# Performance work log

Hardware: AMD Instinct MI355X
Metric: run time of the kernel (lower is better)

The kernel has to match this reference:

```python
import jax, jax.numpy as jnp
import numpy as np

B, H, W, C_IN = 16, 32, 32, 2048
C_PROJ = 2048          # hard-coded Conv2D filters in the module
D_Q = 512              # queries last dim
A = 64                 # num_attributes


def setup_inputs() -> dict:
    key = jax.random.key(0)
    ks = jax.random.split(key, 8)
    s = lambda fan_in: 1.0 / np.sqrt(fan_in)
    return {
        "queries": jax.random.normal(ks[0], (B, C_PROJ, D_Q), jnp.float32),
        "features": jax.random.normal(ks[1], (B, H, W, C_IN), jnp.float32),
        # Dense(num_attributes) on queries
        "Wq": jax.random.normal(ks[2], (D_Q, A), jnp.float32) * s(D_Q),
        "bq": jnp.zeros((A,), jnp.float32),
        # Conv2D 1x1 -> 2048 (feature_transform)
        "Wf": jax.random.normal(ks[3], (C_IN, C_PROJ), jnp.float32) * s(C_IN),
        "bf": jnp.zeros((C_PROJ,), jnp.float32),
        # Conv2D 1x1 -> 2048 (feature_transform1)
        "Wf1": jax.random.normal(ks[4], (C_IN, C_PROJ), jnp.float32) * s(C_IN),
        "bf1": jnpp if False else jnp.zeros((C_PROJ,), jnp.float32),
    }


def reference(queries, features, Wq, bq, Wf, bf, Wf1, bf1):
    # Q: [B, C_PROJ, A]
    Q = jnp.einsum("bcd,da->bca", queries, Wq) + bq
    # 1x1 convs are per-pixel linear maps: [B, H, W, C_PROJ]
    F = jnp.einsum("bhwc,cf->bhwf", features, Wf) + bf
    S = jnp.einsum("bhwc,cf->bhwf", features, Wf1) + bf1
    b, h, w, c = F.shape
    F_new = F.reshape(b, h * w, c)                      # [B, HW, C]
    scale = 1.0 / jnp.sqrt(jnp.float32(A))
    # scores: [B, HW, A]; softmax over attribute axis
    attn = jax.nn.softmax(jnp.einsum("bnc,bca->bna", F_new, Q) * scale, axis=-1)
    attention_map = attn.reshape(b, h, w, A)
    S_flat = S.reshape(b, h * w, c)                     # [B, HW, C]
    # readout: S^T @ attn -> [B, C, A]
    out = jnp.einsum("bnc,bna->bca", S_flat, attn)
    return attention_map, out
```

## Files before the change

kernel.cpp:

```cpp
#include <hip/hip_runtime.h>
#include <math.h>


#define CCH 2048
#define HWD 1024
#define BAD 1024
#define DQD 512
#define NA  64

typedef __attribute__((ext_vector_type(8))) short bf16x8;
typedef __attribute__((ext_vector_type(4))) float f32x4;
typedef __attribute__((ext_vector_type(4))) unsigned short us4;
typedef __attribute__((ext_vector_type(8))) unsigned short us8;

__device__ __forceinline__ unsigned short bfhi(float v) {
    return (unsigned short)(__float_as_uint(v) >> 16);
}
__device__ __forceinline__ float bfres(float v) {
    return v - __uint_as_float(__float_as_uint(v) & 0xffff0000u);
}
__device__ __forceinline__ float bf2f(unsigned short h) {
    return __uint_as_float(((unsigned)h) << 16);
}

__global__ __launch_bounds__(256) void k_convWq(const float* __restrict__ Wq,
    unsigned short* __restrict__ hi, unsigned short* __restrict__ lo)
{
    __shared__ float t[64][65];
    const int tid = threadIdx.x;
    const int k0 = blockIdx.x * 64;
#pragma unroll
    for (int r = 0; r < 4; ++r) {
        int kr = (tid >> 4) + r * 16;
        int cc = (tid & 15) * 4;
        float4 v = *(const float4*)&Wq[(size_t)(k0 + kr) * NA + cc];
        t[kr][cc] = v.x; t[kr][cc + 1] = v.y; t[kr][cc + 2] = v.z; t[kr][cc + 3] = v.w;
    }
    __syncthreads();
#pragma unroll
    for (int r = 0; r < 2; ++r) {
        int a = (tid >> 3) + r * 32;
        int g = tid & 7;
        us8 h8, l8;
#pragma unroll
        for (int j = 0; j < 8; ++j) {
            float v = t[g * 8 + j][a];
            h8[j] = bfhi(v); l8[j] = bfhi(bfres(v));
        }
        *(us8*)&hi[(size_t)a * DQD + k0 + g * 8] = h8;
        *(us8*)&lo[(size_t)a * DQD + k0 + g * 8] = l8;
    }
}

template <int EPI>
__global__ __launch_bounds__(256) void k_gemm_A32(
    const float* __restrict__ A,
    const unsigned short* __restrict__ Bh, const unsigned short* __restrict__ Bl,
    const float* __restrict__ bias,
    unsigned short* __restrict__ Oh, unsigned short* __restrict__ Ol,
    int K, int ldb)
{
    __shared__ unsigned short AsH[4][64][8], AsL[4][64][8], BsH[4][64][8], BsL[4][64][8];
    const int tid = threadIdx.x;
    const int m0 = blockIdx.x * 64, gy = blockIdx.y;
    const int w = tid >> 6, l = tid & 63, lr = l & 15, lg = l >> 4;
    const int sm = tid >> 2, sk = tid & 3, kq = sk * 4;

    const float* pA = A + (size_t)(m0 + sm) * K;
    const unsigned short* pBh = Bh + (size_t)(gy * 64 + sm) * ldb + sk * 8;
    const unsigned short* pBl = Bl + (size_t)(gy * 64 + sm) * ldb + sk * 8;

    f32x4 acc[4] = {{0.f,0.f,0.f,0.f},{0.f,0.f,0.f,0.f},{0.f,0.f,0.f,0.f},{0.f,0.f,0.f,0.f}};

    for (int k0 = 0; k0 < K; k0 += 32) {
        float4 a0 = *(const float4*)&pA[k0 + kq];
        float4 a1 = *(const float4*)&pA[k0 + 16 + kq];
        uint4 vbh = *(const uint4*)pBh; uint4 vbl = *(const uint4*)pBl;
        pBh += 32; pBl += 32;
        us4 h0, l0, h1, l1;
        float a0r[4] = {a0.x, a0.y, a0.z, a0.w}, a1r[4] = {a1.x, a1.y, a1.z, a1.w};
#pragma unroll
        for (int j = 0; j < 4; ++j) {
            h0[j] = bfhi(a0r[j]); l0[j] = bfhi(bfres(a0r[j]));
            h1[j] = bfhi(a1r[j]); l1[j] = bfhi(bfres(a1r[j]));
        }
        __syncthreads();
        *(us4*)&AsH[kq >> 3][sm][kq & 7] = h0;
        *(us4*)&AsL[kq >> 3][sm][kq & 7] = l0;
        *(us4*)&AsH[2 + (kq >> 3)][sm][kq & 7] = h1;
        *(us4*)&AsL[2 + (kq >> 3)][sm][kq & 7] = l1;
        *(uint4*)&BsH[sk][sm][0] = vbh;
        *(uint4*)&BsL[sk][sm][0] = vbl;
        __syncthreads();
        bf16x8 afh = *(const bf16x8*)&AsH[lg][w * 16 + lr][0];
        bf16x8 afl = *(const bf16x8*)&AsL[lg][w * 16 + lr][0];
#pragma unroll
        for (int nt = 0; nt < 4; ++nt) {
            bf16x8 bfh = *(const bf16x8*)&BsH[lg][nt * 16 + lr][0];
            bf16x8 bfl = *(const bf16x8*)&BsL[lg][nt * 16 + lr][0];
            acc[nt] = __builtin_amdgcn_mfma_f32_16x16x32_bf16(afh, bfh, acc[nt], 0, 0, 0);
            acc[nt] = __builtin_amdgcn_mfma_f32_16x16x32_bf16(afh, bfl, acc[nt], 0, 0, 0);
            acc[nt] = __builtin_amdgcn_mfma_f32_16x16x32_bf16(afl, bfh, acc[nt], 0, 0, 0);
        }
    }

    const int mrow0 = m0 + w * 16 + lg * 4;
    if (EPI == 0) {
#pragma unroll
        for (int nt = 0; nt < 4; ++nt) {
            int nn = gy * 64 + nt * 16 + lr;
            us4 h, lo;
#pragma unroll
            for (int j = 0; j < 4; ++j) {
                float v = acc[nt][j];
                h[j] = bfhi(v); lo[j] = bfhi(bfres(v));
            }
            *(us4*)&Oh[(size_t)nn * CCH + mrow0] = h;
            *(us4*)&Ol[(size_t)nn * CCH + mrow0] = lo;
        }
    } else {
        const int b = mrow0 >> 11, cp = mrow0 & 2047;
#pragma unroll
        for (int nt = 0; nt < 4; ++nt) {
            int nloc = nt * 16 + lr;
            float bb = bias[nloc];
            int row = b * 64 + nloc;
            us4 h, lo;
#pragma unroll
            for (int j = 0; j < 4; ++j) {
                float v = acc[nt][j] + bb;
                h[j] = bfhi(v); lo[j] = bfhi(bfres(v));
            }
            *(us4*)&Oh[(size_t)row * CCH + cp] = h;
            *(us4*)&Ol[(size_t)row * CCH + cp] = lo;
        }
    }
}

__global__ __launch_bounds__(256) void k_bq(const unsigned short* __restrict__ QTh,
    const unsigned short* __restrict__ QTl, const float* __restrict__ bf,
    float* __restrict__ bQ)
{
    const int row = blockIdx.x, tid = threadIdx.x;
    us8 h = *(const us8*)(QTh + (size_t)row * CCH + tid * 8);
    us8 l = *(const us8*)(QTl + (size_t)row * CCH + tid * 8);
    float s = 0.f;
#pragma unroll
    for (int j = 0; j < 8; ++j)
        s = fmaf(bf2f(h[j]) + bf2f(l[j]), bf[tid * 8 + j], s);
#pragma unroll
    for (int off = 1; off < 64; off <<= 1) s += __shfl_xor(s, off);
    __shared__ float ps[4];
    if ((tid & 63) == 0) ps[tid >> 6] = s;
    __syncthreads();
    if (tid == 0) bQ[row] = ps[0] + ps[1] + ps[2] + ps[3];
}

__global__ __launch_bounds__(256) void k_scores(
    const float* __restrict__ feat,
    const unsigned short* __restrict__ FQh, const unsigned short* __restrict__ FQl,
    const float* __restrict__ bQ, float* __restrict__ attn,
    unsigned short* __restrict__ ATh, unsigned short* __restrict__ ATl)
{
    __shared__ unsigned short AsH[4][64][8], AsL[4][64][8], BsH[4][64][8], BsL[4][64][8];
    const int tid = threadIdx.x;
    const int b = blockIdx.y, n0 = blockIdx.x * 64;
    const int w = tid >> 6, l = tid & 63, lr = l & 15, lg = l >> 4;
    const int sm = tid >> 2, sk = tid & 3, kq = sk * 4;

    const float* fb = feat + ((size_t)b * HWD + n0) * CCH;
    const unsigned short* pBh = FQh + (size_t)(b * 64 + sm) * CCH + sk * 8;
    const unsigned short* pBl = FQl + (size_t)(b * 64 + sm) * CCH + sk * 8;

    f32x4 acc[4] = {{0.f,0.f,0.f,0.f},{0.f,0.f,0.f,0.f},{0.f,0.f,0.f,0.f},{0.f,0.f,0.f,0.f}};

    for (int k0 = 0; k0 < CCH; k0 += 32) {
        float4 a0 = *(const float4*)&fb[(size_t)sm * CCH + k0 + kq];
        float4 a1 = *(const float4*)&fb[(size_t)sm * CCH + k0 + 16 + kq];
        uint4 vbh = *(const uint4*)pBh; uint4 vbl = *(const uint4*)pBl;
        pBh += 32; pBl += 32;
        us4 h0, l0, h1, l1;
        float a0r[4] = {a0.x, a0.y, a0.z, a0.w}, a1r[4] = {a1.x, a1.y, a1.z, a1.w};
#pragma unroll
        for (int j = 0; j < 4; ++j) {
            h0[j] = bfhi(a0r[j]); l0[j] = bfhi(bfres(a0r[j]));
            h1[j] = bfhi(a1r[j]); l1[j] = bfhi(bfres(a1r[j]));
        }
        __syncthreads();
        *(us4*)&AsH[kq >> 3][sm][kq & 7] = h0;
        *(us4*)&AsL[kq >> 3][sm][kq & 7] = l0;
        *(us4*)&AsH[2 + (kq >> 3)][sm][kq & 7] = h1;
        *(us4*)&AsL[2 + (kq >> 3)][sm][kq & 7] = l1;
        *(uint4*)&BsH[sk][sm][0] = vbh;
        *(uint4*)&BsL[sk][sm][0] = vbl;
        __syncthreads();
        bf16x8 afh = *(const bf16x8*)&AsH[lg][w * 16 + lr][0];
        bf16x8 afl = *(const bf16x8*)&AsL[lg][w * 16 + lr][0];
#pragma unroll
        for (int nt = 0; nt < 4; ++nt) {
            bf16x8 bfh = *(const bf16x8*)&BsH[lg][nt * 16 + lr][0];
            bf16x8 bfl = *(const bf16x8*)&BsL[lg][nt * 16 + lr][0];
            acc[nt] = __builtin_amdgcn_mfma_f32_16x16x32_bf16(afh, bfh, acc[nt], 0, 0, 0);
            acc[nt] = __builtin_amdgcn_mfma_f32_16x16x32_bf16(afh, bfl, acc[nt], 0, 0, 0);
            acc[nt] = __builtin_amdgcn_mfma_f32_16x16x32_bf16(afl, bfh, acc[nt], 0, 0, 0);
        }
    }

    float bq4[4];
#pragma unroll
    for (int nt = 0; nt < 4; ++nt) bq4[nt] = bQ[b * NA + nt * 16 + lr];
#pragma unroll
    for (int j = 0; j < 4; ++j) {
        float v[4];
#pragma unroll
        for (int nt = 0; nt < 4; ++nt) v[nt] = (acc[nt][j] + bq4[nt]) * 0.125f;
        float m = fmaxf(fmaxf(v[0], v[1]), fmaxf(v[2], v[3]));
        m = fmaxf(m, __shfl_xor(m, 1));
        m = fmaxf(m, __shfl_xor(m, 2));
        m = fmaxf(m, __shfl_xor(m, 4));
        m = fmaxf(m, __shfl_xor(m, 8));
        float e[4], s = 0.f;
#pragma unroll
        for (int nt = 0; nt < 4; ++nt) { e[nt] = expf(v[nt] - m); s += e[nt]; }
        s += __shfl_xor(s, 1);
        s += __shfl_xor(s, 2);
        s += __shfl_xor(s, 4);
        s += __shfl_xor(s, 8);
        float inv = 1.f / s;
        const int nr = n0 + w * 16 + lg * 4 + j;
#pragma unroll
        for (int nt = 0; nt < 4; ++nt) {
            float av = e[nt] * inv;
            attn[((size_t)b * HWD + nr) * NA + nt * 16 + lr] = av;
            size_t trow = (size_t)(b * 64 + nt * 16 + lr) * HWD + nr;
            ATh[trow] = bfhi(av);
            ATl[trow] = bfhi(bfres(av));
        }
    }
}

__global__ __launch_bounds__(256) void k_lsum1(const float* __restrict__ attn,
                                               float* __restrict__ part)
{
    const int g = blockIdx.x, b = blockIdx.y;
    const int a = threadIdx.x & 63, q = threadIdx.x >> 6;
    float s = 0.f;
#pragma unroll 4
    for (int n = g * 64 + q * 16; n < g * 64 + q * 16 + 16; ++n)
        s += attn[((size_t)b * HWD + n) * NA + a];
    __shared__ float p[4][64];
    p[q][a] = s;
    __syncthreads();
    if (q == 0) part[(size_t)g * BAD + b * NA + a] = p[0][a] + p[1][a] + p[2][a] + p[3][a];
}

__global__ __launch_bounds__(64) void k_lsum2(const float* __restrict__ part,
                                              float* __restrict__ L)
{
    int ba = blockIdx.x * 64 + threadIdx.x;
    float s = 0.f;
#pragma unroll
    for (int g = 0; g < 16; ++g) s += part[(size_t)g * BAD + ba];
    L[ba] = s;
}

template <int EPI>
__global__ __launch_bounds__(256) void k_gemm_T(
    const float* __restrict__ G,
    const unsigned short* __restrict__ Bh, const unsigned short* __restrict__ Bl,
    unsigned short* __restrict__ Oh, unsigned short* __restrict__ Ol,
    float* __restrict__ Ofp, const float* __restrict__ bias, const float* __restrict__ Lv,
    int K, int ldg, int ldb, long gslab)
{
    __shared__ float At[2048];
    __shared__ unsigned short BsH[4][64][8], BsL[4][64][8];
    const int tid = threadIdx.x;
    const int m0 = blockIdx.x * 64, gy = blockIdx.y;
    const int w = tid >> 6, l = tid & 63, lr = l & 15, lg = l >> 4;
    const int sm = tid >> 2, sk = tid & 3;
    const int kr = tid >> 3, c8 = (tid & 7) * 8;
    const int wkey = (kr >> 3) << 4;
    const int acol = ((w ^ lg) << 4) | lr;

    const float* Gb = G + (size_t)gy * gslab;
    const unsigned short* pBh = Bh + (size_t)(gy * 64 + sm) * ldb + sk * 8;
    const unsigned short* pBl = Bl + (size_t)(gy * 64 + sm) * ldb + sk * 8;

    f32x4 acc[4] = {{0.f,0.f,0.f,0.f},{0.f,0.f,0.f,0.f},{0.f,0.f,0.f,0.f},{0.f,0.f,0.f,0.f}};

    for (int k0 = 0; k0 < K; k0 += 32) {
        float4 g0 = *(const float4*)&Gb[(size_t)(k0 + kr) * ldg + m0 + c8];
        float4 g1 = *(const float4*)&Gb[(size_t)(k0 + kr) * ldg + m0 + c8 + 4];
        uint4 vbh = *(const uint4*)pBh; uint4 vbl = *(const uint4*)pBl;
        pBh += 32; pBl += 32;
        __syncthreads();
        *(float4*)&At[kr * 64 + (c8 ^ wkey)] = g0;
        *(float4*)&At[kr * 64 + (c8 ^ wkey) + 4] = g1;
        *(uint4*)&BsH[sk][sm][0] = vbh;
        *(uint4*)&BsL[sk][sm][0] = vbl;
        __syncthreads();
        bf16x8 afh, afl;
#pragma unroll
        for (int j = 0; j < 8; ++j) {
            float v = At[(lg * 8 + j) * 64 + acol];
            afh[j] = (short)bfhi(v);
            afl[j] = (short)bfhi(bfres(v));
        }
#pragma unroll
        for (int nt = 0; nt < 4; ++nt) {
            bf16x8 bfh = *(const bf16x8*)&BsH[lg][nt * 16 + lr][0];
            bf16x8 bfl = *(const bf16x8*)&BsL[lg][nt * 16 + lr][0];
            acc[nt] = __builtin_amdgcn_mfma_f32_16x16x32_bf16(afh, bfh, acc[nt], 0, 0, 0);
            acc[nt] = __builtin_amdgcn_mfma_f32_16x16x32_bf16(afh, bfl, acc[nt], 0, 0, 0);
            acc[nt] = __builtin_amdgcn_mfma_f32_16x16x32_bf16(afl, bfh, acc[nt], 0, 0, 0);
        }
    }

    const int mrow0 = m0 + w * 16 + lg * 4;
    if (EPI == 0) {
#pragma unroll
        for (int nt = 0; nt < 4; ++nt) {
            int nn = gy * 64 + nt * 16 + lr;
            us4 h, lo;
#pragma unroll
            for (int j = 0; j < 4; ++j) {
                float v = acc[nt][j];
                h[j] = bfhi(v); lo[j] = bfhi(bfres(v));
            }
            *(us4*)&Oh[(size_t)nn * CCH + mrow0] = h;
            *(us4*)&Ol[(size_t)nn * CCH + mrow0] = lo;
        }
    } else {
        float bv[4];
#pragma unroll
        for (int j = 0; j < 4; ++j) bv[j] = bias[mrow0 + j];
#pragma unroll
        for (int nt = 0; nt < 4; ++nt) {
            int nn = gy * 64 + nt * 16 + lr;
            float lb = Lv[nn];
            size_t base = (size_t)(nn >> 6) * (CCH * NA) + (size_t)(nn & 63);
#pragma unroll
            for (int j = 0; j < 4; ++j)
                Ofp[base + (size_t)(mrow0 + j) * NA] = fmaf(bv[j], lb, acc[nt][j]);
        }
    }
}

extern "C" void kernel_launch(void* const* d_in, const int* in_sizes, int n_in,
                              void* d_out, int out_size, void* d_ws, size_t ws_size,
                              hipStream_t stream)
{
    (void)in_sizes; (void)n_in; (void)out_size; (void)ws_size;
    const float* queries  = (const float*)d_in[0];
    const float* features = (const float*)d_in[1];
    const float* Wq  = (const float*)d_in[2];
    const float* bq  = (const float*)d_in[3];
    const float* Wf  = (const float*)d_in[4];
    const float* bf  = (const float*)d_in[5];
    const float* Wf1 = (const float*)d_in[6];
    const float* bf1 = (const float*)d_in[7];
    float* out = (float*)d_out;
    char*  W   = (char*)d_ws;

    unsigned short* QTh = (unsigned short*)(W);
    unsigned short* QTl = (unsigned short*)(W + (4u << 20));
    unsigned short* FQh = (unsigned short*)(W + (8u << 20));
    unsigned short* FQl = (unsigned short*)(W + (12u << 20));
    unsigned short* WqTh = (unsigned short*)(W + (16u << 20));
    unsigned short* WqTl = (unsigned short*)(W + (16u << 20) + (64u << 10));
    float* bQ   = (float*)(W + (16u << 20) + (128u << 10));
    float* L    = (float*)(W + (16u << 20) + (128u << 10) + 4096);
    float* part = (float*)(W + (16u << 20) + (128u << 10) + 8192);
    unsigned short* ATh = QTh;
    unsigned short* ATl = (unsigned short*)(W + (2u << 20));
    unsigned short* TTh = FQh;
    unsigned short* TTl = FQl;

    float* attn = out;
    float* outm = out + 1048576;

    k_convWq<<<dim3(8), 256, 0, stream>>>(Wq, WqTh, WqTl);
    k_gemm_A32<1><<<dim3(512, 1), 256, 0, stream>>>(queries, WqTh, WqTl, bq, QTh, QTl,
                                                    DQD, DQD);
    k_bq<<<dim3(1024), 256, 0, stream>>>(QTh, QTl, bf, bQ);
    k_gemm_A32<0><<<dim3(32, 16), 256, 0, stream>>>(Wf, QTh, QTl, nullptr, FQh, FQl,
                                                    CCH, CCH);
    k_scores<<<dim3(16, 16), 256, 0, stream>>>(features, FQh, FQl, bQ, attn, ATh, ATl);
    k_lsum1<<<dim3(16, 16), 256, 0, stream>>>(attn, part);
    k_lsum2<<<dim3(16), 64, 0, stream>>>(part, L);
    k_gemm_T<0><<<dim3(32, 16), 256, 0, stream>>>(features, ATh, ATl, TTh, TTl,
                                                  nullptr, nullptr, nullptr,
                                                  HWD, CCH, HWD, (long)HWD * CCH);
    k_gemm_T<1><<<dim3(32, 16), 256, 0, stream>>>(Wf1, TTh, TTl, nullptr, nullptr,
                                                  outm, bf1, L,
                                                  CCH, CCH, CCH, 0L);
}
```

Baseline: 489.1 us.

## Restructure GEMM pipeline with pre-split weights, split-K, and separate softmax

Every GEMM stage is rewritten. Wf and Wf1 are converted to hi/lo bf16 up front, and Wf1 is also transposed. The big weight GEMMs now use split-K into fp32 partials, loading operands directly from global memory without LDS, with small combine kernels afterwards. The scores GEMM is split along K, and the softmax plus the attention transpose and sum moves into its own kernel. The T GEMM uses a double-buffered LDS tile with smaller tiles to raise occupancy. The aim is to cut the per-iteration conversion work and barrier syncs and to put more blocks in flight, at the cost of extra partial-buffer traffic and more kernel launches.

```diff
diff --git a/kernel.cpp b/kernel.cpp
--- a/kernel.cpp
+++ b/kernel.cpp
@@ -4,7 +4,6 @@
 
 #define CCH 2048
 #define HWD 1024
-#define BAD 1024
 #define DQD 512
 #define NA  64
 
@@ -21,6 +20,50 @@
 }
 __device__ __forceinline__ float bf2f(unsigned short h) {
     return __uint_as_float(((unsigned)h) << 16);
+}
+
+#define MFMA(A, B, C) __builtin_amdgcn_mfma_f32_16x16x32_bf16((A), (B), (C), 0, 0, 0)
+
+__global__ __launch_bounds__(256) void k_convWf(const float* __restrict__ in,
+    unsigned short* __restrict__ hi, unsigned short* __restrict__ lo)
+{
+    int i = blockIdx.x * 256 + threadIdx.x;
+    float4 v = ((const float4*)in)[i];
+    us4 h, l;
+    float a[4] = {v.x, v.y, v.z, v.w};
+#pragma unroll
+    for (int j = 0; j < 4; ++j) { h[j] = bfhi(a[j]); l[j] = bfhi(bfres(a[j])); }
+    ((us4*)hi)[i] = h;
+    ((us4*)lo)[i] = l;
+}
+
+__global__ __launch_bounds__(256) void k_convT(const float* __restrict__ in,
+    unsigned short* __restrict__ hi, unsigned short* __restrict__ lo)
+{
+    __shared__ float t[64][65];
+    const int tid = threadIdx.x;
+    const int f0 = blockIdx.x * 64, c0 = blockIdx.y * 64;
+#pragma unroll
+    for (int r = 0; r < 4; ++r) {
+        int fr = (tid >> 4) + r * 16;
+        int cc = (tid & 15) * 4;
+        float4 v = *(const float4*)&in[(size_t)(f0 + fr) * CCH + c0 + cc];
+        t[fr][cc] = v.x; t[fr][cc + 1] = v.y; t[fr][cc + 2] = v.z; t[fr][cc + 3] = v.w;
+    }
+    __syncthreads();
+#pragma unroll
+    for (int r = 0; r < 2; ++r) {
+        int c = (tid >> 3) + r * 32;
+        int g = tid & 7;
+        us8 h8, l8;
+#pragma unroll
+        for (int j = 0; j < 8; ++j) {
+            float v = t[g * 8 + j][c];
+            h8[j] = bfhi(v); l8[j] = bfhi(bfres(v));
+        }
+        *(us8*)&hi[(size_t)(c0 + c) * CCH + f0 + g * 8] = h8;
+        *(us8*)&lo[(size_t)(c0 + c) * CCH + f0 + g * 8] = l8;
+    }
 }
 
 __global__ __launch_bounds__(256) void k_convWq(const float* __restrict__ Wq,
@@ -53,87 +96,200 @@
 }
 
 template <int EPI>
-__global__ __launch_bounds__(256) void k_gemm_A32(
-    const float* __restrict__ A,
+__global__ __launch_bounds__(256) void k_gemm_ks(
+    const unsigned short* __restrict__ Ah, const unsigned short* __restrict__ Al,
     const unsigned short* __restrict__ Bh, const unsigned short* __restrict__ Bl,
-    const float* __restrict__ bias,
-    unsigned short* __restrict__ Oh, unsigned short* __restrict__ Ol,
-    int K, int ldb)
-{
-    __shared__ unsigned short AsH[4][64][8], AsL[4][64][8], BsH[4][64][8], BsL[4][64][8];
-    const int tid = threadIdx.x;
-    const int m0 = blockIdx.x * 64, gy = blockIdx.y;
-    const int w = tid >> 6, l = tid & 63, lr = l & 15, lg = l >> 4;
-    const int sm = tid >> 2, sk = tid & 3, kq = sk * 4;
-
-    const float* pA = A + (size_t)(m0 + sm) * K;
-    const unsigned short* pBh = Bh + (size_t)(gy * 64 + sm) * ldb + sk * 8;
-    const unsigned short* pBl = Bl + (size_t)(gy * 64 + sm) * ldb + sk * 8;
-
-    f32x4 acc[4] = {{0.f,0.f,0.f,0.f},{0.f,0.f,0.f,0.f},{0.f,0.f,0.f,0.f},{0.f,0.f,0.f,0.f}};
-
-    for (int k0 = 0; k0 < K; k0 += 32) {
-        float4 a0 = *(const float4*)&pA[k0 + kq];
-        float4 a1 = *(const float4*)&pA[k0 + 16 + kq];
-        uint4 vbh = *(const uint4*)pBh; uint4 vbl = *(const uint4*)pBl;
-        pBh += 32; pBl += 32;
-        us4 h0, l0, h1, l1;
-        float a0r[4] = {a0.x, a0.y, a0.z, a0.w}, a1r[4] = {a1.x, a1.y, a1.z, a1.w};
+    float* __restrict__ P)
+{
+    const int tid = threadIdx.x, w = tid >> 6, l = tid & 63, lr = l & 15, lg = l >> 4;
+    const int wm = w & 1, wn = w >> 1;
+    const int m0 = blockIdx.x * 64 + wm * 32;
+    const int n0 = blockIdx.y * 128 + wn * 64;
+    const int koff = blockIdx.z * 1024;
+    float* Pz = P + (size_t)blockIdx.z * (2048u * 1024u);
+
+    const bf16x8* pA0h = (const bf16x8*)(Ah + (size_t)(m0 + lr) * CCH + koff) + lg;
+    const bf16x8* pA0l = (const bf16x8*)(Al + (size_t)(m0 + lr) * CCH + koff) + lg;
+    const bf16x8* pA1h = (const bf16x8*)(Ah + (size_t)(m0 + 16 + lr) * CCH + koff) + lg;
+    const bf16x8* pA1l = (const bf16x8*)(Al + (size_t)(m0 + 16 + lr) * CCH + koff) + lg;
+    const bf16x8* pBh[4];
+    const bf16x8* pBl[4];
+#pragma unroll
+    for (int nf = 0; nf < 4; ++nf) {
+        pBh[nf] = (const bf16x8*)(Bh + (size_t)(n0 + nf * 16 + lr) * CCH + koff) + lg;
+        pBl[nf] = (const bf16x8*)(Bl + (size_t)(n0 + nf * 16 + lr) * CCH + koff) + lg;
+    }
+
+    f32x4 acc[2][4];
+#pragma unroll
+    for (int mi = 0; mi < 2; ++mi)
+#pragma unroll
+        for (int nf = 0; nf < 4; ++nf) acc[mi][nf] = (f32x4){0.f, 0.f, 0.f, 0.f};
+
+#pragma unroll 2
+    for (int it = 0; it < 32; ++it) {
+        bf16x8 a0h = *pA0h, a0l = *pA0l, a1h = *pA1h, a1l = *pA1l;
+        pA0h += 4; pA0l += 4; pA1h += 4; pA1l += 4;
+#pragma unroll
+        for (int nf = 0; nf < 4; ++nf) {
+            bf16x8 bh = *pBh[nf], bl = *pBl[nf];
+            pBh[nf] += 4; pBl[nf] += 4;
+            acc[0][nf] = MFMA(a0h, bh, acc[0][nf]);
+            acc[0][nf] = MFMA(a0h, bl, acc[0][nf]);
+            acc[0][nf] = MFMA(a0l, bh, acc[0][nf]);
+            acc[1][nf] = MFMA(a1h, bh, acc[1][nf]);
+            acc[1][nf] = MFMA(a1h, bl, acc[1][nf]);
+            acc[1][nf] = MFMA(a1l, bh, acc[1][nf]);
+        }
+    }
+
+#pragma unroll
+    for (int mi = 0; mi < 2; ++mi) {
+        const int mrow0 = m0 + mi * 16 + lg * 4;
+#pragma unroll
+        for (int nf = 0; nf < 4; ++nf) {
+            const int nn = n0 + nf * 16 + lr;
+            if (EPI == 0) {
+                *(f32x4*)&Pz[(size_t)nn * CCH + mrow0] = acc[mi][nf];
+            } else {
+#pragma unroll
+                for (int j = 0; j < 4; ++j)
+                    Pz[(size_t)(mrow0 + j) * 1024 + nn] = acc[mi][nf][j];
+            }
+        }
+    }
+}
+
+__global__ __launch_bounds__(256) void k_fqcomb(const float* __restrict__ P,
+    unsigned short* __restrict__ FQh, unsigned short* __restrict__ FQl)
+{
+    int i = blockIdx.x * 256 + threadIdx.x;
+    float4 v0 = ((const float4*)P)[i];
+    float4 v1 = ((const float4*)P)[i + 524288];
+    us4 h, l;
+    float a[4] = {v0.x + v1.x, v0.y + v1.y, v0.z + v1.z, v0.w + v1.w};
+#pragma unroll
+    for (int j = 0; j < 4; ++j) { h[j] = bfhi(a[j]); l[j] = bfhi(bfres(a[j])); }
+    ((us4*)FQh)[i] = h;
+    ((us4*)FQl)[i] = l;
+}
+
+__global__ __launch_bounds__(256) void k_outcomb(const float* __restrict__ P,
+    const float* __restrict__ bf1, const float* __restrict__ Lv,
+    float* __restrict__ outm)
+{
+    int idx = blockIdx.x * 256 + threadIdx.x;
+    int c = idx >> 8;
+    int ba0 = (idx & 255) * 4;
+    float4 v0 = *(const float4*)&P[(size_t)c * 1024 + ba0];
+    float4 v1 = *(const float4*)&P[2097152u + (size_t)c * 1024 + ba0];
+    float4 lv = *(const float4*)&Lv[ba0];
+    float bb = bf1[c];
+    float4 o;
+    o.x = v0.x + v1.x + bb * lv.x;
+    o.y = v0.y + v1.y + bb * lv.y;
+    o.z = v0.z + v1.z + bb * lv.z;
+    o.w = v0.w + v1.w + bb * lv.w;
+    *(float4*)&outm[(size_t)(ba0 >> 6) * (CCH * NA) + (size_t)c * NA + (ba0 & 63)] = o;
+}
+
+__global__ __launch_bounds__(256) void k_qproj(
+    const float* __restrict__ A, const unsigned short* __restrict__ Bh,
+    const unsigned short* __restrict__ Bl, const float* __restrict__ bq,
+    unsigned short* __restrict__ Oh, unsigned short* __restrict__ Ol)
+{
+    const int tid = threadIdx.x, w = tid >> 6, l = tid & 63, lr = l & 15, lg = l >> 4;
+    const int m16 = w & 1, n32 = w >> 1;
+    const int m0 = blockIdx.x * 32;
+
+    const float* pA = A + (size_t)(m0 + m16 * 16 + lr) * DQD + lg * 8;
+    const size_t br0 = n32 * 32 + lr;
+    const bf16x8* pB0h = (const bf16x8*)(Bh + br0 * DQD) + lg;
+    const bf16x8* pB0l = (const bf16x8*)(Bl + br0 * DQD) + lg;
+    const bf16x8* pB1h = (const bf16x8*)(Bh + (br0 + 16) * DQD) + lg;
+    const bf16x8* pB1l = (const bf16x8*)(Bl + (br0 + 16) * DQD) + lg;
+
+    f32x4 acc0 = {0.f, 0.f, 0.f, 0.f}, acc1 = {0.f, 0.f, 0.f, 0.f};
+#pragma unroll 2
+    for (int it = 0; it < 16; ++it) {
+        float4 a0 = *(const float4*)pA;
+        float4 a1 = *(const float4*)(pA + 4);
+        pA += 32;
+        bf16x8 ah, al_;
+        float ar[8] = {a0.x, a0.y, a0.z, a0.w, a1.x, a1.y, a1.z, a1.w};
+#pragma unroll
+        for (int j = 0; j < 8; ++j) {
+            ah[j] = (short)bfhi(ar[j]); al_[j] = (short)bfhi(bfres(ar[j]));
+        }
+        bf16x8 b0h = *pB0h, b0l = *pB0l;
+        bf16x8 b1h = *pB1h, b1l = *pB1l;
+        pB0h += 4; pB0l += 4; pB1h += 4; pB1l += 4;
+        acc0 = MFMA(ah, b0h, acc0); acc0 = MFMA(ah, b0l, acc0); acc0 = MFMA(al_, b0h, acc0);
+        acc1 = MFMA(ah, b1h, acc1); acc1 = MFMA(ah, b1l, acc1); acc1 = MFMA(al_, b1h, acc1);
+    }
+
+    const int mrow0 = m0 + m16 * 16 + lg * 4;
+    const int b = mrow0 >> 11, cp0 = mrow0 & 2047;
+#pragma unroll
+    for (int nt = 0; nt < 2; ++nt) {
+        f32x4 a = nt ? acc1 : acc0;
+        int ac = n32 * 32 + nt * 16 + lr;
+        float bb = bq[ac];
+        us4 h, lo;
 #pragma unroll
         for (int j = 0; j < 4; ++j) {
-            h0[j] = bfhi(a0r[j]); l0[j] = bfhi(bfres(a0r[j]));
-            h1[j] = bfhi(a1r[j]); l1[j] = bfhi(bfres(a1r[j]));
-        }
-        __syncthreads();
-        *(us4*)&AsH[kq >> 3][sm][kq & 7] = h0;
-        *(us4*)&AsL[kq >> 3][sm][kq & 7] = l0;
-        *(us4*)&AsH[2 + (kq >> 3)][sm][kq & 7] = h1;
-        *(us4*)&AsL[2 + (kq >> 3)][sm][kq & 7] = l1;
-        *(uint4*)&BsH[sk][sm][0] = vbh;
-        *(uint4*)&BsL[sk][sm][0] = vbl;
-        __syncthreads();
-        bf16x8 afh = *(const bf16x8*)&AsH[lg][w * 16 + lr][0];
-        bf16x8 afl = *(const bf16x8*)&AsL[lg][w * 16 + lr][0];
-#pragma unroll
-        for (int nt = 0; nt < 4; ++nt) {
-            bf16x8 bfh = *(const bf16x8*)&BsH[lg][nt * 16 + lr][0];
-            bf16x8 bfl = *(const bf16x8*)&BsL[lg][nt * 16 + lr][0];
-            acc[nt] = __builtin_amdgcn_mfma_f32_16x16x32_bf16(afh, bfh, acc[nt], 0, 0, 0);
-            acc[nt] = __builtin_amdgcn_mfma_f32_16x16x32_bf16(afh, bfl, acc[nt], 0, 0, 0);
-            acc[nt] = __builtin_amdgcn_mfma_f32_16x16x32_bf16(afl, bfh, acc[nt], 0, 0, 0);
-        }
-    }
-
-    const int mrow0 = m0 + w * 16 + lg * 4;
-    if (EPI == 0) {
-#pragma unroll
-        for (int nt = 0; nt < 4; ++nt) {
-            int nn = gy * 64 + nt * 16 + lr;
-            us4 h, lo;
-#pragma unroll
-            for (int j = 0; j < 4; ++j) {
-                float v = acc[nt][j];
-                h[j] = bfhi(v); lo[j] = bfhi(bfres(v));
-            }
-            *(us4*)&Oh[(size_t)nn * CCH + mrow0] = h;
-            *(us4*)&Ol[(size_t)nn * CCH + mrow0] = lo;
-        }
-    } else {
-        const int b = mrow0 >> 11, cp = mrow0 & 2047;
-#pragma unroll
-        for (int nt = 0; nt < 4; ++nt) {
-            int nloc = nt * 16 + lr;
-            float bb = bias[nloc];
-            int row = b * 64 + nloc;
-            us4 h, lo;
-#pragma unroll
-            for (int j = 0; j < 4; ++j) {
-                float v = acc[nt][j] + bb;
-                h[j] = bfhi(v); lo[j] = bfhi(bfres(v));
-            }
-            *(us4*)&Oh[(size_t)row * CCH + cp] = h;
-            *(us4*)&Ol[(size_t)row * CCH + cp] = lo;
-        }
+            float v = a[j] + bb;
+            h[j] = bfhi(v); lo[j] = bfhi(bfres(v));
+        }
+        *(us4*)&Oh[(size_t)(b * 64 + ac) * CCH + cp0] = h;
+        *(us4*)&Ol[(size_t)(b * 64 + ac) * CCH + cp0] = lo;
+    }
+}
+
+__global__ __launch_bounds__(256) void k_scoremm(
+    const float* __restrict__ feat, const unsigned short* __restrict__ FQh,
+    const unsigned short* __restrict__ FQl, float* __restrict__ sp)
+{
+    const int tid = threadIdx.x, w = tid >> 6, l = tid & 63, lr = l & 15, lg = l >> 4;
+    const int m16 = w & 1, n32 = w >> 1;
+    const int m0 = blockIdx.x * 32, b = blockIdx.y, ks = blockIdx.z;
+    const int koff = ks * 1024;
+
+    const float* pA = feat + ((size_t)b * HWD + m0 + m16 * 16 + lr) * CCH + koff + lg * 8;
+    const size_t br0 = (size_t)b * 64 + n32 * 32 + lr;
+    const bf16x8* pB0h = (const bf16x8*)(FQh + br0 * CCH + koff) + lg;
+    const bf16x8* pB0l = (const bf16x8*)(FQl + br0 * CCH + koff) + lg;
+    const bf16x8* pB1h = (const bf16x8*)(FQh + (br0 + 16) * CCH + koff) + lg;
+    const bf16x8* pB1l = (const bf16x8*)(FQl + (br0 + 16) * CCH + koff) + lg;
+
+    f32x4 acc0 = {0.f, 0.f, 0.f, 0.f}, acc1 = {0.f, 0.f, 0.f, 0.f};
+#pragma unroll 2
+    for (int it = 0; it < 32; ++it) {
+        float4 a0 = *(const float4*)pA;
+        float4 a1 = *(const float4*)(pA + 4);
+        pA += 32;
+        bf16x8 ah, al_;
+        float ar[8] = {a0.x, a0.y, a0.z, a0.w, a1.x, a1.y, a1.z, a1.w};
+#pragma unroll
+        for (int j = 0; j < 8; ++j) {
+            ah[j] = (short)bfhi(ar[j]); al_[j] = (short)bfhi(bfres(ar[j]));
+        }
+        bf16x8 b0h = *pB0h, b0l = *pB0l;
+        bf16x8 b1h = *pB1h, b1l = *pB1l;
+        pB0h += 4; pB0l += 4; pB1h += 4; pB1l += 4;
+        acc0 = MFMA(ah, b0h, acc0); acc0 = MFMA(ah, b0l, acc0); acc0 = MFMA(al_, b0h, acc0);
+        acc1 = MFMA(ah, b1h, acc1); acc1 = MFMA(ah, b1l, acc1); acc1 = MFMA(al_, b1h, acc1);
+    }
+
+    float* spb = sp + ((size_t)(ks * 16 + b)) * (HWD * NA);
+    const int nrow0 = m0 + m16 * 16 + lg * 4;
+#pragma unroll
+    for (int nt = 0; nt < 2; ++nt) {
+        f32x4 a = nt ? acc1 : acc0;
+        int ac = n32 * 32 + nt * 16 + lr;
+#pragma unroll
+        for (int j = 0; j < 4; ++j)
+            spb[(size_t)(nrow0 + j) * NA + ac] = a[j];
     }
 }
 
@@ -156,102 +312,78 @@
     if (tid == 0) bQ[row] = ps[0] + ps[1] + ps[2] + ps[3];
 }
 
-__global__ __launch_bounds__(256) void k_scores(
-    const float* __restrict__ feat,
-    const unsigned short* __restrict__ FQh, const unsigned short* __restrict__ FQl,
-    const float* __restrict__ bQ, float* __restrict__ attn,
-    unsigned short* __restrict__ ATh, unsigned short* __restrict__ ATl)
-{
-    __shared__ unsigned short AsH[4][64][8], AsL[4][64][8], BsH[4][64][8], BsL[4][64][8];
-    const int tid = threadIdx.x;
-    const int b = blockIdx.y, n0 = blockIdx.x * 64;
-    const int w = tid >> 6, l = tid & 63, lr = l & 15, lg = l >> 4;
-    const int sm = tid >> 2, sk = tid & 3, kq = sk * 4;
-
-    const float* fb = feat + ((size_t)b * HWD + n0) * CCH;
-    const unsigned short* pBh = FQh + (size_t)(b * 64 + sm) * CCH + sk * 8;
-    const unsigned short* pBl = FQl + (size_t)(b * 64 + sm) * CCH + sk * 8;
-
-    f32x4 acc[4] = {{0.f,0.f,0.f,0.f},{0.f,0.f,0.f,0.f},{0.f,0.f,0.f,0.f},{0.f,0.f,0.f,0.f}};
-
-    for (int k0 = 0; k0 < CCH; k0 += 32) {
-        float4 a0 = *(const float4*)&fb[(size_t)sm * CCH + k0 + kq];
-        float4 a1 = *(const float4*)&fb[(size_t)sm * CCH + k0 + 16 + kq];
-        uint4 vbh = *(const uint4*)pBh; uint4 vbl = *(const uint4*)pBl;
-        pBh += 32; pBl += 32;
-        us4 h0, l0, h1, l1;
-        float a0r[4] = {a0.x, a0.y, a0.z, a0.w}, a1r[4] = {a1.x, a1.y, a1.z, a1.w};
-#pragma unroll
-        for (int j = 0; j < 4; ++j) {
-            h0[j] = bfhi(a0r[j]); l0[j] = bfhi(bfres(a0r[j]));
-            h1[j] = bfhi(a1r[j]); l1[j] = bfhi(bfres(a1r[j]));
-        }
+__global__ __launch_bounds__(256) void k_softmax(
+    const float* __restrict__ sp, const float* __restrict__ bQ,
+    float* __restrict__ attn, unsigned short* __restrict__ ATh,
+    unsigned short* __restrict__ ATl, float* __restrict__ part)
+{
+    __shared__ unsigned short tH[64][72], tL[64][72];
+    __shared__ float red[4][64];
+    const int tid = threadIdx.x, nc = blockIdx.x, b = blockIdx.y;
+    const int r = tid >> 2, q = tid & 3;
+    const size_t base = (((size_t)b) * HWD + nc * 64 + r) * NA + q * 16;
+    const float* sp0 = sp + base;
+    const float* sp1 = sp + (size_t)16 * HWD * NA + base;
+
+    float v[16];
+#pragma unroll
+    for (int i = 0; i < 4; ++i) {
+        float4 x0 = *(const float4*)(sp0 + i * 4);
+        float4 x1 = *(const float4*)(sp1 + i * 4);
+        float4 bb = *(const float4*)&bQ[b * 64 + q * 16 + i * 4];
+        v[i * 4 + 0] = (x0.x + x1.x + bb.x) * 0.125f;
+        v[i * 4 + 1] = (x0.y + x1.y + bb.y) * 0.125f;
+        v[i * 4 + 2] = (x0.z + x1.z + bb.z) * 0.125f;
+        v[i * 4 + 3] = (x0.w + x1.w + bb.w) * 0.125f;
+    }
+    float m = v[0];
+#pragma unroll
+    for (int i = 1; i < 16; ++i) m = fmaxf(m, v[i]);
+    m = fmaxf(m, __shfl_xor(m, 1));
+    m = fmaxf(m, __shfl_xor(m, 2));
+    float s = 0.f;
+#pragma unroll
+    for (int i = 0; i < 16; ++i) { v[i] = expf(v[i] - m); s += v[i]; }
+    s += __shfl_xor(s, 1);
+    s += __shfl_xor(s, 2);
+    float inv = 1.f / s;
+    const size_t ob = (((size_t)b) * HWD + nc * 64 + r) * NA + q * 16;
+#pragma unroll
+    for (int i = 0; i < 4; ++i) {
+        float4 o;
+        o.x = v[i * 4 + 0] * inv; o.y = v[i * 4 + 1] * inv;
+        o.z = v[i * 4 + 2] * inv; o.w = v[i * 4 + 3] * inv;
+        *(float4*)&attn[ob + i * 4] = o;
+    }
+#pragma unroll
+    for (int i = 0; i < 16; ++i) {
+        float av = v[i] * inv;
+        tH[q * 16 + i][r] = bfhi(av);
+        tL[q * 16 + i][r] = bfhi(bfres(av));
+    }
+    __syncthreads();
+    {
+        int a2 = tid >> 2, seg = (tid & 3) * 16;
+        us8 h0 = *(const us8*)&tH[a2][seg];
+        us8 h1 = *(const us8*)&tH[a2][seg + 8];
+        us8 l0 = *(const us8*)&tL[a2][seg];
+        us8 l1 = *(const us8*)&tL[a2][seg + 8];
+        size_t ro = ((size_t)b * 64 + a2) * HWD + nc * 64 + seg;
+        *(us8*)&ATh[ro] = h0; *(us8*)&ATh[ro + 8] = h1;
+        *(us8*)&ATl[ro] = l0; *(us8*)&ATl[ro + 8] = l1;
+    }
+    {
+        int a3 = tid & 63, q3 = tid >> 6;
+        float sL = 0.f;
+#pragma unroll
+        for (int rr = q3 * 16; rr < q3 * 16 + 16; ++rr)
+            sL += bf2f(tH[a3][rr]) + bf2f(tL[a3][rr]);
+        red[q3][a3] = sL;
         __syncthreads();
-        *(us4*)&AsH[kq >> 3][sm][kq & 7] = h0;
-        *(us4*)&AsL[kq >> 3][sm][kq & 7] = l0;
-        *(us4*)&AsH[2 + (kq >> 3)][sm][kq & 7] = h1;
-        *(us4*)&AsL[2 + (kq >> 3)][sm][kq & 7] = l1;
-        *(uint4*)&BsH[sk][sm][0] = vbh;
-        *(uint4*)&BsL[sk][sm][0] = vbl;
-        __syncthreads();
-        bf16x8 afh = *(const bf16x8*)&AsH[lg][w * 16 + lr][0];
-        bf16x8 afl = *(const bf16x8*)&AsL[lg][w * 16 + lr][0];
-#pragma unroll
-        for (int nt = 0; nt < 4; ++nt) {
-            bf16x8 bfh = *(const bf16x8*)&BsH[lg][nt * 16 + lr][0];
-            bf16x8 bfl = *(const bf16x8*)&BsL[lg][nt * 16 + lr][0];
-            acc[nt] = __builtin_amdgcn_mfma_f32_16x16x32_bf16(afh, bfh, acc[nt], 0, 0, 0);
-            acc[nt] = __builtin_amdgcn_mfma_f32_16x16x32_bf16(afh, bfl, acc[nt], 0, 0, 0);
-            acc[nt] = __builtin_amdgcn_mfma_f32_16x16x32_bf16(afl, bfh, acc[nt], 0, 0, 0);
-        }
-    }
-
-    float bq4[4];
-#pragma unroll
-    for (int nt = 0; nt < 4; ++nt) bq4[nt] = bQ[b * NA + nt * 16 + lr];
-#pragma unroll
-    for (int j = 0; j < 4; ++j) {
-        float v[4];
-#pragma unroll
-        for (int nt = 0; nt < 4; ++nt) v[nt] = (acc[nt][j] + bq4[nt]) * 0.125f;
-        float m = fmaxf(fmaxf(v[0], v[1]), fmaxf(v[2], v[3]));
-        m = fmaxf(m, __shfl_xor(m, 1));
-        m = fmaxf(m, __shfl_xor(m, 2));
-        m = fmaxf(m, __shfl_xor(m, 4));
-        m = fmaxf(m, __shfl_xor(m, 8));
-        float e[4], s = 0.f;
-#pragma unroll
-        for (int nt = 0; nt < 4; ++nt) { e[nt] = expf(v[nt] - m); s += e[nt]; }
-        s += __shfl_xor(s, 1);
-        s += __shfl_xor(s, 2);
-        s += __shfl_xor(s, 4);
-        s += __shfl_xor(s, 8);
-        float inv = 1.f / s;
-        const int nr = n0 + w * 16 + lg * 4 + j;
-#pragma unroll
-        for (int nt = 0; nt < 4; ++nt) {
-            float av = e[nt] * inv;
-            attn[((size_t)b * HWD + nr) * NA + nt * 16 + lr] = av;
-            size_t trow = (size_t)(b * 64 + nt * 16 + lr) * HWD + nr;
-            ATh[trow] = bfhi(av);
-            ATl[trow] = bfhi(bfres(av));
-        }
-    }
-}
-
-__global__ __launch_bounds__(256) void k_lsum1(const float* __restrict__ attn,
-                                               float* __restrict__ part)
-{
-    const int g = blockIdx.x, b = blockIdx.y;
-    const int a = threadIdx.x & 63, q = threadIdx.x >> 6;
-    float s = 0.f;
-#pragma unroll 4
-    for (int n = g * 64 + q * 16; n < g * 64 + q * 16 + 16; ++n)
-        s += attn[((size_t)b * HWD + n) * NA + a];
-    __shared__ float p[4][64];
-    p[q][a] = s;
-    __syncthreads();
-    if (q == 0) part[(size_t)g * BAD + b * NA + a] = p[0][a] + p[1][a] + p[2][a] + p[3][a];
+        if (q3 == 0)
+            part[(size_t)nc * 1024 + b * 64 + a3] =
+                red[0][a3] + red[1][a3] + red[2][a3] + red[3][a3];
+    }
 }
 
 __global__ __launch_bounds__(64) void k_lsum2(const float* __restrict__ part,
@@ -260,89 +392,73 @@
     int ba = blockIdx.x * 64 + threadIdx.x;
     float s = 0.f;
 #pragma unroll
-    for (int g = 0; g < 16; ++g) s += part[(size_t)g * BAD + ba];
+    for (int g = 0; g < 16; ++g) s += part[(size_t)g * 1024 + ba];
     L[ba] = s;
 }
 
-template <int EPI>
-__global__ __launch_bounds__(256) void k_gemm_T(
-    const float* __restrict__ G,
-    const unsigned short* __restrict__ Bh, const unsigned short* __restrict__ Bl,
-    unsigned short* __restrict__ Oh, unsigned short* __restrict__ Ol,
-    float* __restrict__ Ofp, const float* __restrict__ bias, const float* __restrict__ Lv,
-    int K, int ldg, int ldb, long gslab)
-{
-    __shared__ float At[2048];
-    __shared__ unsigned short BsH[4][64][8], BsL[4][64][8];
-    const int tid = threadIdx.x;
-    const int m0 = blockIdx.x * 64, gy = blockIdx.y;
-    const int w = tid >> 6, l = tid & 63, lr = l & 15, lg = l >> 4;
-    const int sm = tid >> 2, sk = tid & 3;
-    const int kr = tid >> 3, c8 = (tid & 7) * 8;
-    const int wkey = (kr >> 3) << 4;
-    const int acol = ((w ^ lg) << 4) | lr;
-
-    const float* Gb = G + (size_t)gy * gslab;
-    const unsigned short* pBh = Bh + (size_t)(gy * 64 + sm) * ldb + sk * 8;
-    const unsigned short* pBl = Bl + (size_t)(gy * 64 + sm) * ldb + sk * 8;
-
-    f32x4 acc[4] = {{0.f,0.f,0.f,0.f},{0.f,0.f,0.f,0.f},{0.f,0.f,0.f,0.f},{0.f,0.f,0.f,0.f}};
-
-    for (int k0 = 0; k0 < K; k0 += 32) {
-        float4 g0 = *(const float4*)&Gb[(size_t)(k0 + kr) * ldg + m0 + c8];
-        float4 g1 = *(const float4*)&Gb[(size_t)(k0 + kr) * ldg + m0 + c8 + 4];
-        uint4 vbh = *(const uint4*)pBh; uint4 vbl = *(const uint4*)pBl;
-        pBh += 32; pBl += 32;
+__global__ __launch_bounds__(256) void k_tmat(
+    const float* __restrict__ feat, const unsigned short* __restrict__ ATh,
+    const unsigned short* __restrict__ ATl,
+    unsigned short* __restrict__ TTh, unsigned short* __restrict__ TTl)
+{
+    __shared__ float At[2][32 * 33];
+    const int tid = threadIdx.x, w = tid >> 6, l = tid & 63, lr = l & 15, lg = l >> 4;
+    const int m16 = w & 1, n32 = w >> 1;
+    const int f0 = blockIdx.x * 32, b = blockIdx.y;
+    const int kr = tid >> 3, c4 = (tid & 7) * 4;
+
+    const float* G = feat + (size_t)b * HWD * CCH;
+    const size_t br0 = (size_t)b * 64 + n32 * 32 + lr;
+    const bf16x8* pB0h = (const bf16x8*)(ATh + br0 * HWD) + lg;
+    const bf16x8* pB0l = (const bf16x8*)(ATl + br0 * HWD) + lg;
+    const bf16x8* pB1h = (const bf16x8*)(ATh + (br0 + 16) * HWD) + lg;
+    const bf16x8* pB1l = (const bf16x8*)(ATl + (br0 + 16) * HWD) + lg;
+
+    f32x4 acc0 = {0.f, 0.f, 0.f, 0.f}, acc1 = {0.f, 0.f, 0.f, 0.f};
+
+    {
+        float4 g = *(const float4*)&G[(size_t)kr * CCH + f0 + c4];
+        At[0][kr * 33 + c4 + 0] = g.x; At[0][kr * 33 + c4 + 1] = g.y;
+        At[0][kr * 33 + c4 + 2] = g.z; At[0][kr * 33 + c4 + 3] = g.w;
+    }
+    int cur = 0;
+    for (int it = 0; it < 32; ++it) {
+        float4 gn = {0.f, 0.f, 0.f, 0.f};
+        if (it < 31)
+            gn = *(const float4*)&G[(size_t)((it + 1) * 32 + kr) * CCH + f0 + c4];
         __syncthreads();
-        *(float4*)&At[kr * 64 + (c8 ^ wkey)] = g0;
-        *(float4*)&At[kr * 64 + (c8 ^ wkey) + 4] = g1;
-        *(uint4*)&BsH[sk][sm][0] = vbh;
-        *(uint4*)&BsL[sk][sm][0] = vbl;
+        float av[8];
+#pragma unroll
+        for (int j = 0; j < 8; ++j)
+            av[j] = At[cur][(lg * 8 + j) * 33 + m16 * 16 + lr];
+        bf16x8 ah, al_;
+#pragma unroll
+        for (int j = 0; j < 8; ++j) {
+            ah[j] = (short)bfhi(av[j]); al_[j] = (short)bfhi(bfres(av[j]));
+        }
+        bf16x8 b0h = *pB0h, b0l = *pB0l;
+        bf16x8 b1h = *pB1h, b1l = *pB1l;
+        pB0h += 4; pB0l += 4; pB1h += 4; pB1l += 4;
+        acc0 = MFMA(ah, b0h, acc0); acc0 = MFMA(ah, b0l, acc0); acc0 = MFMA(al_, b0h, acc0);
+        acc1 = MFMA(ah, b1h, acc1); acc1 = MFMA(ah, b1l, acc1); acc1 = MFMA(al_, b1h, acc1);
         __syncthreads();
-        bf16x8 afh, afl;
-#pragma unroll
-        for (int j = 0; j < 8; ++j) {
-            float v = At[(lg * 8 + j) * 64 + acol];
-            afh[j] = (short)bfhi(v);
-            afl[j] = (short)bfhi(bfres(v));
-        }
-#pragma unroll
-        for (int nt = 0; nt < 4; ++nt) {
-            bf16x8 bfh = *(const bf16x8*)&BsH[lg][nt * 16 + lr][0];
-            bf16x8 bfl = *(const bf16x8*)&BsL[lg][nt * 16 + lr][0];
-            acc[nt] = __builtin_amdgcn_mfma_f32_16x16x32_bf16(afh, bfh, acc[nt], 0, 0, 0);
-            acc[nt] = __builtin_amdgcn_mfma_f32_16x16x32_bf16(afh, bfl, acc[nt], 0, 0, 0);
-            acc[nt] = __builtin_amdgcn_mfma_f32_16x16x32_bf16(afl, bfh, acc[nt], 0, 0, 0);
-        }
-    }
-
-    const int mrow0 = m0 + w * 16 + lg * 4;
-    if (EPI == 0) {
-#pragma unroll
-        for (int nt = 0; nt < 4; ++nt) {
-            int nn = gy * 64 + nt * 16 + lr;
-            us4 h, lo;
-#pragma unroll
-            for (int j = 0; j < 4; ++j) {
-                float v = acc[nt][j];
-                h[j] = bfhi(v); lo[j] = bfhi(bfres(v));
-            }
-            *(us4*)&Oh[(size_t)nn * CCH + mrow0] = h;
-            *(us4*)&Ol[(size_t)nn * CCH + mrow0] = lo;
-        }
-    } else {
-        float bv[4];
-#pragma unroll
-        for (int j = 0; j < 4; ++j) bv[j] = bias[mrow0 + j];
-#pragma unroll
-        for (int nt = 0; nt < 4; ++nt) {
-            int nn = gy * 64 + nt * 16 + lr;
-            float lb = Lv[nn];
-            size_t base = (size_t)(nn >> 6) * (CCH * NA) + (size_t)(nn & 63);
-#pragma unroll
-            for (int j = 0; j < 4; ++j)
-                Ofp[base + (size_t)(mrow0 + j) * NA] = fmaf(bv[j], lb, acc[nt][j]);
-        }
+        if (it < 31) {
+            At[cur ^ 1][kr * 33 + c4 + 0] = gn.x; At[cur ^ 1][kr * 33 + c4 + 1] = gn.y;
+            At[cur ^ 1][kr * 33 + c4 + 2] = gn.z; At[cur ^ 1][kr * 33 + c4 + 3] = gn.w;
+        }
+        cur ^= 1;
+    }
+
+    const int mrow0 = f0 + m16 * 16 + lg * 4;
+#pragma unroll
+    for (int nt = 0; nt < 2; ++nt) {
+        f32x4 a = nt ? acc1 : acc0;
+        int ac = n32 * 32 + nt * 16 + lr;
+        us4 h, lo;
+#pragma unroll
+        for (int j = 0; j < 4; ++j) { h[j] = bfhi(a[j]); lo[j] = bfhi(bfres(a[j])); }
+        *(us4*)&TTh[(size_t)(b * 64 + ac) * CCH + mrow0] = h;
+        *(us4*)&TTl[(size_t)(b * 64 + ac) * CCH + mrow0] = lo;
     }
 }
 
@@ -362,36 +478,41 @@
     float* out = (float*)d_out;
     char*  W   = (char*)d_ws;
 
-    unsigned short* QTh = (unsigned short*)(W);
-    unsigned short* QTl = (unsigned short*)(W + (4u << 20));
-    unsigned short* FQh = (unsigned short*)(W + (8u << 20));
-    unsigned short* FQl = (unsigned short*)(W + (12u << 20));
-    unsigned short* WqTh = (unsigned short*)(W + (16u << 20));
-    unsigned short* WqTl = (unsigned short*)(W + (16u << 20) + (64u << 10));
-    float* bQ   = (float*)(W + (16u << 20) + (128u << 10));
-    float* L    = (float*)(W + (16u << 20) + (128u << 10) + 4096);
-    float* part = (float*)(W + (16u << 20) + (128u << 10) + 8192);
-    unsigned short* ATh = QTh;
-    unsigned short* ATl = (unsigned short*)(W + (2u << 20));
-    unsigned short* TTh = FQh;
-    unsigned short* TTl = FQl;
+    const size_t MB = 1u << 20;
+    unsigned short* QTh  = (unsigned short*)(W);
+    unsigned short* QTl  = (unsigned short*)(W + 4 * MB);
+    unsigned short* FQh  = (unsigned short*)(W + 8 * MB);
+    unsigned short* FQl  = (unsigned short*)(W + 12 * MB);
+    unsigned short* WfH  = (unsigned short*)(W + 16 * MB);
+    unsigned short* WfL  = (unsigned short*)(W + 24 * MB);
+    unsigned short* W1TH = (unsigned short*)(W + 32 * MB);
+    unsigned short* W1TL = (unsigned short*)(W + 40 * MB);
+    unsigned short* TTh  = (unsigned short*)(W + 48 * MB);
+    unsigned short* TTl  = (unsigned short*)(W + 52 * MB);
+    unsigned short* ATh  = (unsigned short*)(W + 56 * MB);
+    unsigned short* ATl  = (unsigned short*)(W + 58 * MB);
+    float* sp   = (float*)(W + 60 * MB);
+    float* P    = (float*)(W + 68 * MB);
+    unsigned short* WqTh = (unsigned short*)(W + 84 * MB);
+    unsigned short* WqTl = (unsigned short*)(W + 84 * MB + 65536);
+    float* bQ   = (float*)(W + 84 * MB + 131072);
+    float* L    = (float*)(W + 84 * MB + 131072 + 4096);
+    float* part = (float*)(W + 84 * MB + 131072 + 8192);
 
     float* attn = out;
     float* outm = out + 1048576;
 
+    k_convWf<<<dim3(4096), 256, 0, stream>>>(Wf, WfH, WfL);
+    k_convT <<<dim3(32, 32), 256, 0, stream>>>(Wf1, W1TH, W1TL);
     k_convWq<<<dim3(8), 256, 0, stream>>>(Wq, WqTh, WqTl);
-    k_gemm_A32<1><<<dim3(512, 1), 256, 0, stream>>>(queries, WqTh, WqTl, bq, QTh, QTl,
-                                                    DQD, DQD);
+    k_qproj<<<dim3(1024), 256, 0, stream>>>(queries, WqTh, WqTl, bq, QTh, QTl);
     k_bq<<<dim3(1024), 256, 0, stream>>>(QTh, QTl, bf, bQ);
-    k_gemm_A32<0><<<dim3(32, 16), 256, 0, stream>>>(Wf, QTh, QTl, nullptr, FQh, FQl,
-                                                    CCH, CCH);
-    k_scores<<<dim3(16, 16), 256, 0, stream>>>(features, FQh, FQl, bQ, attn, ATh, ATl);
-    k_lsum1<<<dim3(16, 16), 256, 0, stream>>>(attn, part);
+    k_gemm_ks<0><<<dim3(32, 8, 2), 256, 0, stream>>>(WfH, WfL, QTh, QTl, P);
+    k_fqcomb<<<dim3(2048), 256, 0, stream>>>(P, FQh, FQl);
+    k_scoremm<<<dim3(32, 16, 2), 256, 0, stream>>>(features, FQh, FQl, sp);
+    k_softmax<<<dim3(16, 16), 256, 0, stream>>>(sp, bQ, attn, ATh, ATl, part);
     k_lsum2<<<dim3(16), 64, 0, stream>>>(part, L);
-    k_gemm_T<0><<<dim3(32, 16), 256, 0, stream>>>(features, ATh, ATl, TTh, TTl,
-                                                  nullptr, nullptr, nullptr,
-                                                  HWD, CCH, HWD, (long)HWD * CCH);
-    k_gemm_T<1><<<dim3(32, 16), 256, 0, stream>>>(Wf1, TTh, TTl, nullptr, nullptr,
-                                                  outm, bf1, L,
-                                                  CCH, CCH, CCH, 0L);
-}
+    k_tmat<<<dim3(64, 16), 256, 0, stream>>>(features, ATh, ATl, TTh, TTl);
+    k_gemm_ks<1><<<dim3(32, 8, 2), 256, 0, stream>>>(W1TH, W1TL, TTh, TTl, P);
+    k_outcomb<<<dim3(2048), 256, 0, stream>>>(P, bf1, L, outm);
+}
```

New measurement: 646.9 us. 32.3% more time.
